# Performance work log

Hardware: AMD Instinct MI355X
Metric: run time of the kernel (lower is better)

Reference implementation:

```python
import jax, jax.numpy as jnp
import numpy as np

G, NPG, MAXN = 1024, 40, 51   # graphs, nodes/graph, dense pad size
EPG = 80                       # edges per graph
N, E = G * NPG, G * EPG
D_IN, D_OUT, D_EDGE = 64, 32, 16


def _lin(key, fan_in, shape):
    b = 1.0 / np.sqrt(fan_in)
    return jax.random.uniform(key, shape, jnp.float32, -b, b)


def setup_inputs() -> dict:
    key = jax.random.key(0)
    ks = jax.random.split(key, 24)
    node_features = jax.random.randint(ks[0], (N, 9), 0, 128)
    edge_features = jax.random.randint(ks[1], (E, 3), 0, 8)
    offs = jnp.repeat(jnp.arange(G) * NPG, EPG)
    src = jax.random.randint(ks[2], (E,), 0, NPG) + offs
    dst = jax.random.randint(ks[3], (E,), 0, NPG) + offs
    edge_index = jnp.stack([src, dst])
    batch = jnp.repeat(jnp.arange(G), NPG)
    inp = dict(node_features=node_features, edge_features=edge_features,
               edge_index=edge_index, batch=batch)
    # OGB-style encoders: one embedding table per feature column, summed
    inp['atom_emb'] = jax.random.normal(ks[4], (9, 128, D_IN), jnp.float32) * 0.1
    inp['bond_emb'] = jax.random.normal(ks[5], (3, 8, D_EDGE), jnp.float32) * 0.1
    # edge-conditioned weight MLP: 16 -> 1024 -> 256 -> 64*32 (no bias)
    inp['gW1'] = _lin(ks[6], 16, (16, 1024))
    inp['gW2'] = _lin(ks[7], 1024, (1024, 256))
    inp['gW3'] = _lin(ks[8], 256, (256, D_IN * D_OUT))
    # NNConv root weight + bias
    inp['root'] = _lin(ks[9], D_IN, (D_IN, D_OUT))
    inp['conv_bias'] = jnp.zeros((D_OUT,), jnp.float32)
    # readout MLP: 51*32 -> 256 -> 128 -> 32 -> 8 -> 1
    dims = [MAXN * D_OUT, 256, 128, 32, 8, 1]
    for i in range(5):
        inp[f'mW{i+1}'] = _lin(ks[10 + 2 * i], dims[i], (dims[i], dims[i + 1]))
        inp[f'mb{i+1}'] = _lin(ks[11 + 2 * i], dims[i], (dims[i + 1],))
    return inp


def reference(node_features, edge_features, edge_index, batch,
              atom_emb, bond_emb, gW1, gW2, gW3, root, conv_bias,
              mW1, mb1, mW2, mb2, mW3, mb3, mW4, mb4, mW5, mb5):
    # encoders: sum of per-column embeddings
    x = jnp.sum(atom_emb[jnp.arange(9), node_features], axis=1)      # [N,64]
    e = jnp.sum(bond_emb[jnp.arange(3), edge_features], axis=1)      # [E,16]
    # per-edge weight matrix via MLP
    h = jax.nn.relu(e @ gW1)
    h = jax.nn.relu(h @ gW2)
    w = (h @ gW3).reshape(-1, D_IN, D_OUT)                           # [E,64,32]
    # NNConv: gather src, per-edge matmul, scatter-add to dst, + root + bias
    src, dst = edge_index[0], edge_index[1]
    msg = jnp.einsum('ed,edo->eo', x[src], w)                        # [E,32]
    agg = jax.ops.segment_sum(msg, dst, num_segments=N)              # [N,32]
    out = agg + x @ root + conv_bias
    # to_dense_batch(max_num_nodes=51); exactly NPG nodes per graph, zero-pad
    dense = jnp.zeros((G, MAXN, D_OUT), out.dtype).at[:, :NPG].set(
        out.reshape(G, NPG, D_OUT))
    f = dense.reshape(G, MAXN * D_OUT)                               # [G,1632]
    f = jax.nn.relu(f @ mW1 + mb1)
    f = jax.nn.relu(f @ mW2 + mb2)
    f = jax.nn.relu(f @ mW3 + mb3)
    f = jax.nn.relu(f @ mW4 + mb4)
    return f @ mW5 + mb5                                             # [G,1]
```

## Files before the change

kernel.cpp:

```cpp
#include <hip/hip_runtime.h>

#define NNODES 40960
#define NEDGES 81920
#define NG     1024
#define NCOMBO 512

__global__ __launch_bounds__(256) void k_node(
    const int* __restrict__ nf, const float* __restrict__ emb,
    const float* __restrict__ root, const float* __restrict__ bias,
    float* __restrict__ x, float* __restrict__ out) {
    __shared__ float sx[4][64];
    const int t = threadIdx.x;
    const int ln = t >> 6;
    const int d  = t & 63;
    const int n  = blockIdx.x * 4 + ln;
    const int* nfr = nf + n * 9;
    float acc = 0.f;
#pragma unroll
    for (int c = 0; c < 9; ++c) {
        int idx = nfr[c];
        acc += emb[((c << 7) + idx) * 64 + d];
    }
    x[n * 64 + d] = acc;
    sx[ln][d] = acc;
    __syncthreads();
    if (d < 32) {
        float o = bias[d];
#pragma unroll
        for (int k = 0; k < 64; ++k) o += sx[ln][k] * root[k * 32 + d];
        out[n * 32 + d] = o;
    }
}

__global__ __launch_bounds__(256) void k_h1(
    const float* __restrict__ bemb, const float* __restrict__ gW1,
    float* __restrict__ h1) {
    __shared__ float se[16];
    const int b = blockIdx.x, t = threadIdx.x;
    const int c = b >> 2;
    const int n = ((b & 3) << 8) + t;
    if (t < 16) {
        int f0 = c >> 6, f1 = (c >> 3) & 7, f2 = c & 7;
        se[t] = bemb[f0 * 16 + t] + bemb[(8 + f1) * 16 + t] +
                bemb[(16 + f2) * 16 + t];
    }
    __syncthreads();
    float acc = 0.f;
#pragma unroll
    for (int k = 0; k < 16; ++k) acc += se[k] * gW1[k * 1024 + n];
    h1[c * 1024 + n] = fmaxf(acc, 0.f);
}

template <int BM, int BN, int BK, int TM, int TN>
__global__ __launch_bounds__(256)
void k_gemm_tiled(const float* __restrict__ A, const float* __restrict__ B,
                  const float* __restrict__ bias, float* __restrict__ C,
                  float* __restrict__ Cp, int M, int N, int K, int KS, int relu) {
    constexpr int TX = BN / TN;
    constexpr int TY = BM / TM;
    static_assert(TX * TY == 256, "block must be 256 threads");
    __shared__ float As[BK][BM + 4];
    __shared__ float Bs[BK][BN + 4];
    const int tx = threadIdx.x % TX, ty = threadIdx.x / TX;
    const int row0 = blockIdx.y * BM, col0 = blockIdx.x * BN;
    const int z = blockIdx.z;
    const int k_begin = z * KS, k_end = k_begin + KS;

    const int am = threadIdx.x >> 2;
    const int ak = (threadIdx.x & 3) << 2;
    const int bk = threadIdx.x >> 4;
    const int bn = (threadIdx.x & 15) << 2;

    float acc[TM][TN] = {};
    for (int k0 = k_begin; k0 < k_end; k0 += BK) {
        float4 av = *reinterpret_cast<const float4*>(&A[(row0 + am) * K + k0 + ak]);
        float4 bv = *reinterpret_cast<const float4*>(&B[(k0 + bk) * N + col0 + bn]);
        As[ak + 0][am] = av.x;
        As[ak + 1][am] = av.y;
        As[ak + 2][am] = av.z;
        As[ak + 3][am] = av.w;
        *reinterpret_cast<float4*>(&Bs[bk][bn]) = bv;
        __syncthreads();
#pragma unroll
        for (int k = 0; k < BK; ++k) {
            float a[TM], b[TN];
            *reinterpret_cast<float4*>(a) =
                *reinterpret_cast<const float4*>(&As[k][ty * TM]);
            *reinterpret_cast<float4*>(b) =
                *reinterpret_cast<const float4*>(&Bs[k][tx * TN]);
#pragma unroll
            for (int i = 0; i < TM; ++i)
#pragma unroll
                for (int j = 0; j < TN; ++j) acc[i][j] += a[i] * b[j];
        }
        __syncthreads();
    }

    const int MN = M * N;
    if (gridDim.z == 1) {
#pragma unroll
        for (int i = 0; i < TM; ++i) {
            int r = row0 + ty * TM + i;
            float4 v;
            v.x = acc[i][0]; v.y = acc[i][1]; v.z = acc[i][2]; v.w = acc[i][3];
            int c = col0 + tx * TN;
            if (bias) { v.x += bias[c]; v.y += bias[c+1]; v.z += bias[c+2]; v.w += bias[c+3]; }
            if (relu) { v.x = fmaxf(v.x,0.f); v.y = fmaxf(v.y,0.f);
                        v.z = fmaxf(v.z,0.f); v.w = fmaxf(v.w,0.f); }
            *reinterpret_cast<float4*>(&C[r * N + c]) = v;
        }
    } else {
        float* dstp = Cp + z * MN;
#pragma unroll
        for (int i = 0; i < TM; ++i) {
            int r = row0 + ty * TM + i;
            float4 v;
            v.x = acc[i][0]; v.y = acc[i][1]; v.z = acc[i][2]; v.w = acc[i][3];
            *reinterpret_cast<float4*>(&dstp[r * N + col0 + tx * TN]) = v;
        }
    }
}

__global__ void k_reduceK(const float* __restrict__ Cp, const float* __restrict__ bias,
                          float* __restrict__ C, int MN, int N, int nz, int relu) {
    int i4 = (blockIdx.x * 256 + threadIdx.x) * 4;
    if (i4 >= MN) return;
    float4 acc = *reinterpret_cast<const float4*>(&Cp[i4]);
    for (int z = 1; z < nz; ++z) {
        float4 t = *reinterpret_cast<const float4*>(&Cp[z * MN + i4]);
        acc.x += t.x; acc.y += t.y; acc.z += t.z; acc.w += t.w;
    }
    if (bias) {
        int c = i4 % N;
        acc.x += bias[c]; acc.y += bias[c + 1]; acc.z += bias[c + 2]; acc.w += bias[c + 3];
    }
    if (relu) {
        acc.x = fmaxf(acc.x, 0.f); acc.y = fmaxf(acc.y, 0.f);
        acc.z = fmaxf(acc.z, 0.f); acc.w = fmaxf(acc.w, 0.f);
    }
    *reinterpret_cast<float4*>(&C[i4]) = acc;
}

__global__ void k_msg(const float* __restrict__ x, const float* __restrict__ wtab,
                      const int* __restrict__ ef, const int* __restrict__ src,
                      const int* __restrict__ dst, float* __restrict__ out) {
    int gid = blockIdx.x * blockDim.x + threadIdx.x;
    int e = gid >> 5, o = gid & 31;
    int s = src[e], d = dst[e];
    int c = (ef[e * 3] << 6) | (ef[e * 3 + 1] << 3) | ef[e * 3 + 2];
    const float* xr = x + s * 64;
    const float* w = wtab + c * 2048 + o;
    float acc = 0.f;
#pragma unroll
    for (int k = 0; k < 64; ++k) acc += xr[k] * w[k * 32];
    atomicAdd(&out[d * 32 + o], acc);
}

__global__ __launch_bounds__(256) void k_tail2(
    const float* __restrict__ f1,
    const float* __restrict__ mW2, const float* __restrict__ mb2,
    const float* __restrict__ mW3, const float* __restrict__ mb3,
    const float* __restrict__ mW4, const float* __restrict__ mb4,
    const float* __restrict__ mW5, const float* __restrict__ mb5,
    float* __restrict__ outv) {
    __shared__ float s1[4][256];
    __shared__ float s2[4][128];
    __shared__ float s3[4][32];
    __shared__ float s4[4][8];
    const int t  = threadIdx.x;
    const int g0 = blockIdx.x * 4;
#pragma unroll
    for (int i = 0; i < 4; ++i) {
        int idx = t + i * 256;
        s1[idx >> 8][idx & 255] = f1[g0 * 256 + idx];
    }
    __syncthreads();
#pragma unroll
    for (int i = 0; i < 2; ++i) {
        int idx = t + i * 256;
        int g = idx >> 7, cc = idx & 127;
        float acc = mb2[cc];
#pragma unroll 8
        for (int k = 0; k < 256; ++k) acc += s1[g][k] * mW2[k * 128 + cc];
        s2[g][cc] = fmaxf(acc, 0.f);
    }
    __syncthreads();
    const int w = t >> 6, lane = t & 63;
    if (lane < 32) {
        float acc = mb3[lane];
#pragma unroll 8
        for (int k = 0; k < 128; ++k) acc += s2[w][k] * mW3[k * 32 + lane];
        s3[w][lane] = fmaxf(acc, 0.f);
    }
    __syncthreads();
    if (lane < 8) {
        float acc = mb4[lane];
#pragma unroll
        for (int k = 0; k < 32; ++k) acc += s3[w][k] * mW4[k * 8 + lane];
        s4[w][lane] = fmaxf(acc, 0.f);
    }
    __syncthreads();
    if (lane == 0) {
        float acc = mb5[0];
#pragma unroll
        for (int k = 0; k < 8; ++k) acc += s4[w][k] * mW5[k];
        outv[g0 + w] = acc;
    }
}

extern "C" void kernel_launch(void* const* d_in, const int* in_sizes, int n_in,
                              void* d_out, int out_size, void* d_ws, size_t ws_size,
                              hipStream_t stream) {
    const int*   nf      = (const int*)d_in[0];
    const int*   ef      = (const int*)d_in[1];
    const int*   eidx    = (const int*)d_in[2];
    const float* atom_emb= (const float*)d_in[4];
    const float* bond_emb= (const float*)d_in[5];
    const float* gW1     = (const float*)d_in[6];
    const float* gW2     = (const float*)d_in[7];
    const float* gW3     = (const float*)d_in[8];
    const float* root    = (const float*)d_in[9];
    const float* cbias   = (const float*)d_in[10];
    const float* mW1     = (const float*)d_in[11];
    const float* mb1     = (const float*)d_in[12];
    const float* mW2     = (const float*)d_in[13];
    const float* mb2     = (const float*)d_in[14];
    const float* mW3     = (const float*)d_in[15];
    const float* mb3     = (const float*)d_in[16];
    const float* mW4     = (const float*)d_in[17];
    const float* mb4     = (const float*)d_in[18];
    const float* mW5     = (const float*)d_in[19];
    const float* mb5     = (const float*)d_in[20];

    const int* src = eidx;
    const int* dst = eidx + NEDGES;

    float* ws = (float*)d_ws;
    float* x    = ws;
    float* out  = x + 2621440;
    float* h1   = out + 1310720;
    float* h2   = h1 + 524288;
    float* wtab = h2 + 131072;
    float* f1   = wtab + 1048576;
    float* part = f1 + 262144;

    k_node<<<NNODES / 4, 256, 0, stream>>>(nf, atom_emb, root, cbias, x, out);
    k_h1<<<NCOMBO * 4, 256, 0, stream>>>(bond_emb, gW1, h1);
    k_gemm_tiled<64, 64, 16, 4, 4><<<dim3(4, 8, 16), 256, 0, stream>>>(
        h1, gW2, nullptr, nullptr, part, NCOMBO, 256, 1024, 64, 0);
    k_reduceK<<<131072 / 1024, 256, 0, stream>>>(part, nullptr, h2, 131072, 256, 16, 1);
    k_gemm_tiled<64, 64, 16, 4, 4><<<dim3(32, 8, 2), 256, 0, stream>>>(
        h2, gW3, nullptr, nullptr, part, NCOMBO, 2048, 256, 128, 0);
    k_reduceK<<<1048576 / 1024, 256, 0, stream>>>(part, nullptr, wtab, 1048576, 2048, 2, 0);
    k_msg<<<NEDGES * 32 / 256, 256, 0, stream>>>(x, wtab, ef, src, dst, out);
    k_gemm_tiled<64, 64, 16, 4, 4><<<dim3(4, 16, 8), 256, 0, stream>>>(
        out, mW1, nullptr, nullptr, part, NG, 256, 1280, 160, 0);
    k_reduceK<<<262144 / 1024, 256, 0, stream>>>(part, mb1, f1, 262144, 256, 8, 1);
    k_tail2<<<NG / 4, 256, 0, stream>>>(f1, mW2, mb2, mW3, mb3, mW4, mb4,
                                        mW5, mb5, (float*)d_out);
}
```

Baseline: 233.8 us.

## Bucket edges by bond combo and reuse per-combo weight matrix in registers

Adds a histogram, a scan and a scatter pass that sort edges by their 512 possible bond-feature combinations. The message kernel then processes one combo per block group: it loads that combo's 64x32 weight matrix into registers once and applies it to up to 64 gathered source rows staged in shared memory. This replaces the old kernel, which re-read the weight matrix from global memory for every edge. The cost is three extra small kernels, including a serial single-block scan, and about 64 registers per thread for the weights.

```diff
diff --git a/kernel.cpp b/kernel.cpp
--- a/kernel.cpp
+++ b/kernel.cpp
@@ -4,6 +4,8 @@
 #define NEDGES 81920
 #define NG     1024
 #define NCOMBO 512
+#define NHB    320
+#define NGRP   4
 
 __global__ __launch_bounds__(256) void k_node(
     const int* __restrict__ nf, const float* __restrict__ emb,
@@ -49,6 +51,58 @@
 #pragma unroll
     for (int k = 0; k < 16; ++k) acc += se[k] * gW1[k * 1024 + n];
     h1[c * 1024 + n] = fmaxf(acc, 0.f);
+}
+
+__global__ void k_hist(const int* __restrict__ ef, int* __restrict__ cid,
+                       int* __restrict__ bh) {
+    __shared__ int lh[512];
+    const int t = threadIdx.x, b = blockIdx.x;
+    lh[t] = 0; lh[t + 256] = 0;
+    __syncthreads();
+    int e = b * 256 + t;
+    int c = (ef[e * 3] << 6) | (ef[e * 3 + 1] << 3) | ef[e * 3 + 2];
+    cid[e] = c;
+    atomicAdd(&lh[c], 1);
+    __syncthreads();
+    bh[b * 512 + t]       = lh[t];
+    bh[b * 512 + 256 + t] = lh[t + 256];
+}
+
+__global__ __launch_bounds__(512) void k_scan(int* __restrict__ bh,
+                                              int* __restrict__ offs) {
+    __shared__ int tmp[512];
+    const int c = threadIdx.x;
+    int s = 0;
+    for (int b = 0; b < NHB; ++b) {
+        int v = bh[b * 512 + c];
+        bh[b * 512 + c] = s;
+        s += v;
+    }
+    tmp[c] = s;
+    __syncthreads();
+    for (int d = 1; d < 512; d <<= 1) {
+        int add = (c >= d) ? tmp[c - d] : 0;
+        __syncthreads();
+        tmp[c] += add;
+        __syncthreads();
+    }
+    int excl = tmp[c] - s;
+    offs[c] = excl;
+    if (c == 511) offs[512] = tmp[511];
+    for (int b = 0; b < NHB; ++b) bh[b * 512 + c] += excl;
+}
+
+__global__ void k_scatter(const int* __restrict__ cid, const int* __restrict__ src,
+                          const int* __restrict__ dst, const int* __restrict__ bh,
+                          int2* __restrict__ esd) {
+    __shared__ int cur[512];
+    const int t = threadIdx.x, b = blockIdx.x;
+    cur[t]       = bh[b * 512 + t];
+    cur[t + 256] = bh[b * 512 + 256 + t];
+    __syncthreads();
+    int e = b * 256 + t;
+    int p = atomicAdd(&cur[cid[e]], 1);
+    esd[p] = make_int2(src[e], dst[e]);
 }
 
 template <int BM, int BN, int BK, int TM, int TN>
@@ -141,19 +195,65 @@
     *reinterpret_cast<float4*>(&C[i4]) = acc;
 }
 
-__global__ void k_msg(const float* __restrict__ x, const float* __restrict__ wtab,
-                      const int* __restrict__ ef, const int* __restrict__ src,
-                      const int* __restrict__ dst, float* __restrict__ out) {
-    int gid = blockIdx.x * blockDim.x + threadIdx.x;
-    int e = gid >> 5, o = gid & 31;
-    int s = src[e], d = dst[e];
-    int c = (ef[e * 3] << 6) | (ef[e * 3 + 1] << 3) | ef[e * 3 + 2];
-    const float* xr = x + s * 64;
-    const float* w = wtab + c * 2048 + o;
-    float acc = 0.f;
-#pragma unroll
-    for (int k = 0; k < 64; ++k) acc += xr[k] * w[k * 32];
-    atomicAdd(&out[d * 32 + o], acc);
+__global__ __launch_bounds__(256) void k_msgg(
+    const float* __restrict__ x, const float* __restrict__ wtab,
+    const int* __restrict__ offs, const int2* __restrict__ esd,
+    float* __restrict__ out) {
+    const int c   = blockIdx.x >> 2;
+    const int grp = blockIdx.x & 3;
+    const int t = threadIdx.x;
+    const int o = t & 31, slot = t >> 5;
+    const int e0 = offs[c];
+    const int n_c = offs[c + 1] - e0;
+    if (grp * 64 >= n_c) return;
+
+    __shared__ float swT[32][65];
+    __shared__ float sx[64][64];
+    __shared__ int ssrc[64], sdst[64];
+
+#pragma unroll
+    for (int j = 0; j < 8; ++j) {
+        int i = t + j * 256;
+        swT[i & 31][i >> 5] = wtab[c * 2048 + i];
+    }
+    __syncthreads();
+    float wr[64];
+#pragma unroll
+    for (int k = 0; k < 64; ++k) wr[k] = swT[o][k];
+
+    for (int base = grp * 64; base < n_c; base += NGRP * 64) {
+        int n_e = min(64, n_c - base);
+        __syncthreads();
+        if (t < n_e) {
+            int2 sd = esd[e0 + base + t];
+            ssrc[t] = sd.x; sdst[t] = sd.y;
+        }
+        __syncthreads();
+#pragma unroll
+        for (int i = 0; i < 16; ++i) {
+            int idx = t + i * 256;
+            int r = idx >> 6, d = idx & 63;
+            if (r < n_e) sx[r][d] = x[ssrc[r] * 64 + d];
+        }
+        __syncthreads();
+#pragma unroll
+        for (int j = 0; j < 8; ++j) {
+            int ei = slot * 8 + j;
+            if (ei < n_e) {
+                const float4* xv = reinterpret_cast<const float4*>(sx[ei]);
+                float acc = 0.f;
+#pragma unroll
+                for (int k4 = 0; k4 < 16; ++k4) {
+                    float4 xq = xv[k4];
+                    acc += xq.x * wr[k4 * 4 + 0];
+                    acc += xq.y * wr[k4 * 4 + 1];
+                    acc += xq.z * wr[k4 * 4 + 2];
+                    acc += xq.w * wr[k4 * 4 + 3];
+                }
+                atomicAdd(&out[sdst[ei] * 32 + o], acc);
+            }
+        }
+    }
 }
 
 __global__ __launch_bounds__(256) void k_tail2(
@@ -243,8 +343,15 @@
     float* wtab = h2 + 131072;
     float* f1   = wtab + 1048576;
     float* part = f1 + 262144;
+    int*   cid  = (int*)(part + 2097152);
+    int*   bh   = cid + 81920;
+    int*   offs = bh + 163840;
+    int2*  esd  = (int2*)(offs + 1024);
 
     k_node<<<NNODES / 4, 256, 0, stream>>>(nf, atom_emb, root, cbias, x, out);
+    k_hist<<<NHB, 256, 0, stream>>>(ef, cid, bh);
+    k_scan<<<1, 512, 0, stream>>>(bh, offs);
+    k_scatter<<<NHB, 256, 0, stream>>>(cid, src, dst, bh, esd);
     k_h1<<<NCOMBO * 4, 256, 0, stream>>>(bond_emb, gW1, h1);
     k_gemm_tiled<64, 64, 16, 4, 4><<<dim3(4, 8, 16), 256, 0, stream>>>(
         h1, gW2, nullptr, nullptr, part, NCOMBO, 256, 1024, 64, 0);
@@ -252,7 +359,7 @@
     k_gemm_tiled<64, 64, 16, 4, 4><<<dim3(32, 8, 2), 256, 0, stream>>>(
         h2, gW3, nullptr, nullptr, part, NCOMBO, 2048, 256, 128, 0);
     k_reduceK<<<1048576 / 1024, 256, 0, stream>>>(part, nullptr, wtab, 1048576, 2048, 2, 0);
-    k_msg<<<NEDGES * 32 / 256, 256, 0, stream>>>(x, wtab, ef, src, dst, out);
+    k_msgg<<<NCOMBO * NGRP, 256, 0, stream>>>(x, wtab, offs, esd, out);
     k_gemm_tiled<64, 64, 16, 4, 4><<<dim3(4, 16, 8), 256, 0, stream>>>(
         out, mW1, nullptr, nullptr, part, NG, 256, 1280, 160, 0);
     k_reduceK<<<262144 / 1024, 256, 0, stream>>>(part, mb1, f1, 262144, 256, 8, 1);
```

New measurement: 268.4 us. 1.15x slower.

## Rewrite edge message kernel with LDS-staged x and pipelined inline-asm weight loads

Applied to the files above, without the earlier changes.

Replaces the per-output-scalar message kernel with one that handles 32 edges per block. Each thread now computes 4 outputs of one edge. Source node rows are staged in shared memory, and the per-edge weight table is streamed with hand-issued dwordx4 global loads in a software pipeline with explicit vmcnt waits, overlapping loads with FMAs. This aims to cut scalar load count and raise memory-level parallelism. In exchange it uses inline asm with fixed offsets and sched barriers, and occupancy may drop because of the added registers.

```diff
diff --git a/kernel.cpp b/kernel.cpp
--- a/kernel.cpp
+++ b/kernel.cpp
@@ -4,6 +4,18 @@
 #define NEDGES 81920
 #define NG     1024
 #define NCOMBO 512
+
+#define ISSUE4(V, p, A0, A1, A2, A3) asm volatile( \
+  "global_load_dwordx4 %0, %4, off offset:" #A0 "\n\t" \
+  "global_load_dwordx4 %1, %4, off offset:" #A1 "\n\t" \
+  "global_load_dwordx4 %2, %4, off offset:" #A2 "\n\t" \
+  "global_load_dwordx4 %3, %4, off offset:" #A3 "\n\t" \
+  : "=v"(V[0]), "=v"(V[1]), "=v"(V[2]), "=v"(V[3]) : "v"(p))
+
+#define WAIT4(N) do { \
+    asm volatile("s_waitcnt vmcnt(" #N ")" ::: "memory"); \
+    __builtin_amdgcn_sched_barrier(0); \
+  } while (0)
 
 __global__ __launch_bounds__(256) void k_node(
     const int* __restrict__ nf, const float* __restrict__ emb,
@@ -141,19 +153,64 @@
     *reinterpret_cast<float4*>(&C[i4]) = acc;
 }
 
-__global__ void k_msg(const float* __restrict__ x, const float* __restrict__ wtab,
-                      const int* __restrict__ ef, const int* __restrict__ src,
-                      const int* __restrict__ dst, float* __restrict__ out) {
-    int gid = blockIdx.x * blockDim.x + threadIdx.x;
-    int e = gid >> 5, o = gid & 31;
-    int s = src[e], d = dst[e];
-    int c = (ef[e * 3] << 6) | (ef[e * 3 + 1] << 3) | ef[e * 3 + 2];
-    const float* xr = x + s * 64;
-    const float* w = wtab + c * 2048 + o;
-    float acc = 0.f;
-#pragma unroll
-    for (int k = 0; k < 64; ++k) acc += xr[k] * w[k * 32];
-    atomicAdd(&out[d * 32 + o], acc);
+__global__ __launch_bounds__(256) void k_msg4a(
+    const float* __restrict__ x, const float* __restrict__ wtab,
+    const int* __restrict__ ef, const int* __restrict__ src,
+    const int* __restrict__ dst, float* __restrict__ out) {
+    __shared__ float sx[32][64];
+    const int t = threadIdx.x;
+    const int e_base = blockIdx.x * 32;
+#pragma unroll
+    for (int i = 0; i < 8; ++i) {
+        int idx = t + i * 256;
+        int r = idx >> 6, cl = idx & 63;
+        sx[r][cl] = x[src[e_base + r] * 64 + cl];
+    }
+    const int slot = t >> 3;
+    const int o4   = (t & 7) << 2;
+    const int e = e_base + slot;
+    const int d = dst[e];
+    const int c = (ef[e * 3] << 6) | (ef[e * 3 + 1] << 3) | ef[e * 3 + 2];
+    const float* wl = wtab + c * 2048 + o4;
+    const float* wh = wl + 1024;
+    __syncthreads();
+
+    float4 W0[4], W1[4], W2[4], W3[4];
+    float4 acc = make_float4(0.f, 0.f, 0.f, 0.f);
+    const float* sxe = sx[slot];
+
+#define FMA4(W, KB) \
+    { _Pragma("unroll") for (int i = 0; i < 4; ++i) { \
+        float q = sxe[(KB) + i]; \
+        acc.x += q * W[i].x; acc.y += q * W[i].y; \
+        acc.z += q * W[i].z; acc.w += q * W[i].w; } }
+
+    ISSUE4(W0, wl, 0, 128, 256, 384);
+    ISSUE4(W1, wl, 512, 640, 768, 896);
+    ISSUE4(W2, wl, 1024, 1152, 1280, 1408);
+    WAIT4(8); ISSUE4(W3, wl, 1536, 1664, 1792, 1920); FMA4(W0, 0);
+    WAIT4(8); ISSUE4(W0, wl, 2048, 2176, 2304, 2432); FMA4(W1, 4);
+    WAIT4(8); ISSUE4(W1, wl, 2560, 2688, 2816, 2944); FMA4(W2, 8);
+    WAIT4(8); ISSUE4(W2, wl, 3072, 3200, 3328, 3456); FMA4(W3, 12);
+    WAIT4(8); ISSUE4(W3, wl, 3584, 3712, 3840, 3968); FMA4(W0, 16);
+    WAIT4(8); ISSUE4(W0, wh, 0, 128, 256, 384);       FMA4(W1, 20);
+    WAIT4(8); ISSUE4(W1, wh, 512, 640, 768, 896);     FMA4(W2, 24);
+    WAIT4(8); ISSUE4(W2, wh, 1024, 1152, 1280, 1408); FMA4(W3, 28);
+    WAIT4(8); ISSUE4(W3, wh, 1536, 1664, 1792, 1920); FMA4(W0, 32);
+    WAIT4(8); ISSUE4(W0, wh, 2048, 2176, 2304, 2432); FMA4(W1, 36);
+    WAIT4(8); ISSUE4(W1, wh, 2560, 2688, 2816, 2944); FMA4(W2, 40);
+    WAIT4(8); ISSUE4(W2, wh, 3072, 3200, 3328, 3456); FMA4(W3, 44);
+    WAIT4(8); ISSUE4(W3, wh, 3584, 3712, 3840, 3968); FMA4(W0, 48);
+    WAIT4(8); FMA4(W1, 52);
+    WAIT4(4); FMA4(W2, 56);
+    WAIT4(0); FMA4(W3, 60);
+#undef FMA4
+
+    float* op = out + d * 32 + o4;
+    atomicAdd(op + 0, acc.x);
+    atomicAdd(op + 1, acc.y);
+    atomicAdd(op + 2, acc.z);
+    atomicAdd(op + 3, acc.w);
 }
 
 __global__ __launch_bounds__(256) void k_tail2(
@@ -252,7 +309,7 @@
     k_gemm_tiled<64, 64, 16, 4, 4><<<dim3(32, 8, 2), 256, 0, stream>>>(
         h2, gW3, nullptr, nullptr, part, NCOMBO, 2048, 256, 128, 0);
     k_reduceK<<<1048576 / 1024, 256, 0, stream>>>(part, nullptr, wtab, 1048576, 2048, 2, 0);
-    k_msg<<<NEDGES * 32 / 256, 256, 0, stream>>>(x, wtab, ef, src, dst, out);
+    k_msg4a<<<NEDGES / 32, 256, 0, stream>>>(x, wtab, ef, src, dst, out);
     k_gemm_tiled<64, 64, 16, 4, 4><<<dim3(4, 16, 8), 256, 0, stream>>>(
         out, mW1, nullptr, nullptr, part, NG, 256, 1280, 160, 0);
     k_reduceK<<<262144 / 1024, 256, 0, stream>>>(part, mb1, f1, 262144, 256, 8, 1);
```

Result: no change. 237.7 us (+1.6%).
